# Kernel optimization log

Measured on AMD Instinct MI355X. Metric: run time of the kernel, lower is better.

## Reference

```python
import jax, jax.numpy as jnp
import numpy as np
import math

B, L, D = 4, 2048, 1024        # batch, x_len, x_dim
QKV, H = 64, 16                # qkv_dim, head_dim (number of heads)


def setup_inputs() -> dict:
    key = jax.random.key(0)
    ks = jax.random.split(key, 10)
    s = 1.0 / math.sqrt(D)
    return {
        "x": jax.random.normal(ks[0], (B, L, D), jnp.float32),
        "encoder_x": jax.random.normal(ks[1], (B, L, D), jnp.float32),
        "Wq": jax.random.normal(ks[2], (D, QKV * H), jnp.float32) * s,
        "bq": jax.random.normal(ks[3], (QKV * H,), jnp.float32) * 0.01,
        "Wk": jax.random.normal(ks[4], (D, QKV * H), jnp.float32) * s,
        "bk": jax.random.normal(ks[5], (QKV * H,), jnp.float32) * 0.01,
        "Wv": jax.random.normal(ks[6], (D, QKV * H), jnp.float32) * s,
        "bv": jax.random.normal(ks[7], (QKV * H,), jnp.float32) * 0.01,
        "Wo": jax.random.normal(ks[8], (QKV * H, D), jnp.float32) * s,
        "bo": jax.random.normal(ks[9], (D,), jnp.float32) * 0.01,
    }


def reference(x, encoder_x, Wq, bq, Wk, bk, Wv, bv, Wo, bo):
    # q,k from encoder_x; v from x  -> [B, L, H, QKV]
    q = (encoder_x @ Wq + bq).reshape(B, L, H, QKV)
    k = (encoder_x @ Wk + bk).reshape(B, L, H, QKV)
    v = (x @ Wv + bv).reshape(B, L, H, QKV)
    # explicit [B,H,L,L] score matrix + softmax over k (faithful to source)
    scores = jax.nn.softmax(
        jnp.einsum("bqhd,bkhd->bhqk", q, k) / math.sqrt(QKV), axis=-1
    )
    # faithful to source einsum 'bvhd,bhqk->bvhd': no shared contraction
    # index, so scores are summed over (q,k) and broadcast onto v per (b,h).
    attn = jnp.einsum("bvhd,bhqk->bvhd", v, scores).reshape(B, L, H * QKV)
    return attn @ Wo + bo
```

## Files before the change

### kernel.cpp

```cpp
#include <hip/hip_runtime.h>
#include <stdint.h>


typedef __attribute__((ext_vector_type(8))) short bf16x8;
typedef __attribute__((ext_vector_type(4))) float f32x4;

typedef __attribute__((address_space(1))) void as1_void;
typedef __attribute__((address_space(3))) void as3_void;
#define GLD16(g, s)                                                          \
  __builtin_amdgcn_global_load_lds((as1_void*)(g), (as3_void*)(s), 16, 0, 0)

__device__ __forceinline__ short f2bf(float f) {
  union { float f; uint32_t u; } v; v.f = f;
  uint32_t r = v.u + 0x7FFFu + ((v.u >> 16) & 1u);
  return (short)(r >> 16);
}

__device__ __forceinline__ bf16x8 pack8(f32x4 a, f32x4 b) {
  union { f32x4 f; uint32_t u[4]; } x, y;
  x.f = a; y.f = b;
#pragma unroll
  for (int t = 0; t < 4; ++t) x.u[t] += 0x8000u;
#pragma unroll
  for (int t = 0; t < 4; ++t) y.u[t] += 0x8000u;
  union { bf16x8 v; uint32_t u[4]; } o;
  o.u[0] = __builtin_amdgcn_perm(x.u[1], x.u[0], 0x07060302);
  o.u[1] = __builtin_amdgcn_perm(x.u[3], x.u[2], 0x07060302);
  o.u[2] = __builtin_amdgcn_perm(y.u[1], y.u[0], 0x07060302);
  o.u[3] = __builtin_amdgcn_perm(y.u[3], y.u[2], 0x07060302);
  return o.v;
}

__global__ __launch_bounds__(256) void cast_f32_bf16(
    const float* __restrict__ in, short* __restrict__ out, int n8) {
  int i = blockIdx.x * blockDim.x + threadIdx.x;
  if (i >= n8) return;
  const float4* p = (const float4*)in;
  float4 a = p[2 * (size_t)i], b = p[2 * (size_t)i + 1];
  bf16x8 o;
  o[0] = f2bf(a.x); o[1] = f2bf(a.y); o[2] = f2bf(a.z); o[3] = f2bf(a.w);
  o[4] = f2bf(b.x); o[5] = f2bf(b.y); o[6] = f2bf(b.z); o[7] = f2bf(b.w);
  *(bf16x8*)(out + 8 * (size_t)i) = o;
}

__global__ __launch_bounds__(256) void transpose_cast(
    const float* __restrict__ in, short* __restrict__ out, int n) {
  __shared__ float tile[64][65];
  const int br = blockIdx.y * 64, bc = blockIdx.x * 64;
  const int tid = threadIdx.x;
#pragma unroll
  for (int t = 0; t < 16; ++t) {
    int idx = t * 256 + tid;
    int r = idx >> 6, c = idx & 63;
    tile[r][c] = in[(size_t)(br + r) * n + bc + c];
  }
  __syncthreads();
#pragma unroll
  for (int t = 0; t < 16; ++t) {
    int idx = t * 256 + tid;
    int r = idx >> 6, c = idx & 63;
    out[(size_t)(bc + r) * n + br + c] = f2bf(tile[c][r]);
  }
}

__global__ __launch_bounds__(256) void bias_fuse(
    const float* __restrict__ bv, const float* __restrict__ Wo,
    const float* __restrict__ bo, float* __restrict__ biasc, int D, int N) {
  __shared__ float red[256];
  const int tid = threadIdx.x;
  const int nx = tid & 15, ky = tid >> 4;
  const int n = blockIdx.x * 16 + nx;
  float s = 0.f;
  for (int k = ky; k < D; k += 16)
    s += bv[k] * Wo[(size_t)k * N + n];
  red[tid] = s;
  __syncthreads();
#pragma unroll
  for (int st = 128; st >= 16; st >>= 1) {
    if (tid < st) red[tid] += red[tid + st];
    __syncthreads();
  }
  if (ky == 0) biasc[n] = 2048.0f * red[nx] + bo[n];
}

__global__ __launch_bounds__(256) void gemm_w(
    const short* __restrict__ Wot, const float* __restrict__ Wv,
    short* __restrict__ Wt, int N, int K) {
  constexpr int BK = 64;
  __shared__ __align__(16) short As[64 * BK];
  __shared__ __align__(16) float Bsf[64 * BK];
  const int tid = threadIdx.x, lane = tid & 63, wave = tid >> 6;
  const int bm = blockIdx.y * 64, bn = blockIdx.x * 64;
  const int wm = (wave >> 1) * 32, wn = (wave & 1) * 32;
  const int l15 = lane & 15, quad = lane >> 4;

  f32x4 acc[2][2];
#pragma unroll
  for (int i = 0; i < 2; ++i)
#pragma unroll
    for (int j = 0; j < 2; ++j) acc[i][j] = (f32x4){0.f, 0.f, 0.f, 0.f};

  const int ar = tid >> 3, ac8 = (tid & 7) ^ (ar & 7);
  const short* pa = Wot + (size_t)(bm + ar) * K + ac8 * 8;
  short* la = As + tid * 8;
  const int br = tid >> 4, bc4 = (tid & 15) ^ (br & 7);
  const float* pb = Wv + (size_t)(bn + br) * K + bc4 * 4;
  float* lb = Bsf + tid * 4;

  for (int kt = 0; kt < K; kt += BK) {
#pragma unroll
    for (int s = 0; s < 2; ++s) GLD16(pa + (size_t)(32 * s) * K, la + 2048 * s);
#pragma unroll
    for (int s = 0; s < 4; ++s) GLD16(pb + (size_t)(16 * s) * K, lb + 1024 * s);
    pa += BK; pb += BK;
    __syncthreads();
#pragma unroll
    for (int kk = 0; kk < 2; ++kk) {
      bf16x8 af[2], bfr[2];
#pragma unroll
      for (int i = 0; i < 2; ++i) {
        const int r = wm + i * 16 + l15;
        af[i] = *(const bf16x8*)(As + r * BK + ((kk * 4 + quad) ^ (r & 7)) * 8);
      }
#pragma unroll
      for (int j = 0; j < 2; ++j) {
        const int r = wn + j * 16 + l15;
        const int c4 = kk * 8 + quad * 2;
        f32x4 u0 = *(const f32x4*)(Bsf + (r * 16 + (c4 ^ (r & 7))) * 4);
        f32x4 u1 = *(const f32x4*)(Bsf + (r * 16 + ((c4 + 1) ^ (r & 7))) * 4);
        bfr[j] = pack8(u0, u1);
      }
#pragma unroll
      for (int i = 0; i < 2; ++i)
#pragma unroll
        for (int j = 0; j < 2; ++j)
          acc[i][j] = __builtin_amdgcn_mfma_f32_16x16x32_bf16(
              af[i], bfr[j], acc[i][j], 0, 0, 0);
    }
    __syncthreads();
  }
#pragma unroll
  for (int j = 0; j < 2; ++j) {
    const int col = bn + wn + j * 16 + l15;
#pragma unroll
    for (int i = 0; i < 2; ++i) {
      const int row0 = bm + wm + i * 16 + quad * 4;
#pragma unroll
      for (int r = 0; r < 4; ++r)
        Wt[(size_t)(row0 + r) * N + col] = f2bf(2048.f * acc[i][j][r]);
    }
  }
}

__global__ __launch_bounds__(256) void gemm_main(
    const short* __restrict__ A, const short* __restrict__ Bt,
    const float* __restrict__ bias, float* __restrict__ Out,
    int M, int N, int K) {
  constexpr int BK = 64;
  __shared__ __align__(16) char smem[24576];
  short* As = (short*)smem;
  short* Bs = (short*)(smem + 16384);
  const int tid = threadIdx.x, lane = tid & 63, wave = tid >> 6;
  const int b = blockIdx.x;
  const int bm = (b & 63) * 128;
  const int bn = (b >> 6) * 64;
  const int wm = (wave & 1) * 64, wn = (wave >> 1) * 32;
  const int l15 = lane & 15, quad = lane >> 4;

  f32x4 acc[4][2];
#pragma unroll
  for (int i = 0; i < 4; ++i)
#pragma unroll
    for (int j = 0; j < 2; ++j) acc[i][j] = (f32x4){0.f, 0.f, 0.f, 0.f};

  const int srow = tid >> 3, sc8 = (tid & 7) ^ (srow & 7);
  const short* pa = A + (size_t)(bm + srow) * K + sc8 * 8;
  const short* pb = Bt + (size_t)(bn + srow) * K + sc8 * 8;
  short* la = As + tid * 8;
  short* lb = Bs + tid * 8;

  for (int kt = 0; kt < K; kt += BK) {
#pragma unroll
    for (int s = 0; s < 4; ++s) GLD16(pa + (size_t)(32 * s) * K, la + 2048 * s);
#pragma unroll
    for (int s = 0; s < 2; ++s) GLD16(pb + (size_t)(32 * s) * K, lb + 2048 * s);
    pa += BK; pb += BK;
    __syncthreads();
#pragma unroll
    for (int kk = 0; kk < 2; ++kk) {
      bf16x8 af[4], bfr[2];
#pragma unroll
      for (int i = 0; i < 4; ++i) {
        const int r = wm + i * 16 + l15;
        af[i] = *(const bf16x8*)(As + r * BK + ((kk * 4 + quad) ^ (r & 7)) * 8);
      }
#pragma unroll
      for (int j = 0; j < 2; ++j) {
        const int r = wn + j * 16 + l15;
        bfr[j] = *(const bf16x8*)(Bs + r * BK + ((kk * 4 + quad) ^ (r & 7)) * 8);
      }
#pragma unroll
      for (int i = 0; i < 4; ++i)
#pragma unroll
        for (int j = 0; j < 2; ++j)
          acc[i][j] = __builtin_amdgcn_mfma_f32_16x16x32_bf16(
              af[i], bfr[j], acc[i][j], 0, 0, 0);
    }
    __syncthreads();
  }

  float* T = (float*)smem + wave * 576;
#pragma unroll
  for (int i = 0; i < 4; ++i) {
#pragma unroll
    for (int j = 0; j < 2; ++j) {
      const float bb = bias[bn + wn + j * 16 + l15];
#pragma unroll
      for (int r = 0; r < 4; ++r)
        T[(quad * 4 + r) * 36 + j * 16 + l15] = acc[i][j][r] + bb;
    }
#pragma unroll
    for (int c = 0; c < 2; ++c) {
      const int row = (lane >> 3) + 8 * c;
      f32x4 v = *(const f32x4*)(T + row * 36 + (lane & 7) * 4);
      *(f32x4*)(Out + (size_t)(bm + wm + i * 16 + row) * N + bn + wn +
                (lane & 7) * 4) = v;
    }
  }
}

extern "C" void kernel_launch(void* const* d_in, const int* in_sizes, int n_in,
                              void* d_out, int out_size, void* d_ws,
                              size_t ws_size, hipStream_t stream) {
  const float* x  = (const float*)d_in[0];
  const float* Wv = (const float*)d_in[6];
  const float* bv = (const float*)d_in[7];
  const float* Wo = (const float*)d_in[8];
  const float* bo = (const float*)d_in[9];
  float* out = (float*)d_out;

  constexpr int L = 2048, D = 1024, NO = 1024;
  constexpr int M = 4 * L;

  char* ws = (char*)d_ws;
  short* x_bf   = (short*)(ws);
  short* wot_bf = (short*)(ws + (16u << 20));
  short* wt_bf  = (short*)(ws + (18u << 20));
  float* biasc  = (float*)(ws + (20u << 20));

  cast_f32_bf16<<<(M * D / 8) / 256, 256, 0, stream>>>(x, x_bf, M * D / 8);
  transpose_cast<<<dim3(16, 16), 256, 0, stream>>>(Wo, wot_bf, NO);
  bias_fuse<<<NO / 16, 256, 0, stream>>>(bv, Wo, bo, biasc, D, NO);
  gemm_w<<<dim3(16, 16), 256, 0, stream>>>(wot_bf, Wv, wt_bf, NO, D);
  gemm_main<<<(M / 128) * (NO / 64), 256, 0, stream>>>(
      x_bf, wt_bf, biasc, out, M, NO, D);
}
```

Before: 185.2 us.

## Merge prep kernels into one launch and halve gemm_w tile height

Result: faster. 181.0 us (-2.3%).

```diff
diff --git a/kernel.cpp b/kernel.cpp
--- a/kernel.cpp
+++ b/kernel.cpp
@@ -31,74 +31,74 @@
   return o.v;
 }
 
-__global__ __launch_bounds__(256) void cast_f32_bf16(
-    const float* __restrict__ in, short* __restrict__ out, int n8) {
-  int i = blockIdx.x * blockDim.x + threadIdx.x;
-  if (i >= n8) return;
-  const float4* p = (const float4*)in;
-  float4 a = p[2 * (size_t)i], b = p[2 * (size_t)i + 1];
-  bf16x8 o;
-  o[0] = f2bf(a.x); o[1] = f2bf(a.y); o[2] = f2bf(a.z); o[3] = f2bf(a.w);
-  o[4] = f2bf(b.x); o[5] = f2bf(b.y); o[6] = f2bf(b.z); o[7] = f2bf(b.w);
-  *(bf16x8*)(out + 8 * (size_t)i) = o;
-}
-
-__global__ __launch_bounds__(256) void transpose_cast(
-    const float* __restrict__ in, short* __restrict__ out, int n) {
-  __shared__ float tile[64][65];
-  const int br = blockIdx.y * 64, bc = blockIdx.x * 64;
-  const int tid = threadIdx.x;
-#pragma unroll
-  for (int t = 0; t < 16; ++t) {
-    int idx = t * 256 + tid;
-    int r = idx >> 6, c = idx & 63;
-    tile[r][c] = in[(size_t)(br + r) * n + bc + c];
-  }
-  __syncthreads();
-#pragma unroll
-  for (int t = 0; t < 16; ++t) {
-    int idx = t * 256 + tid;
-    int r = idx >> 6, c = idx & 63;
-    out[(size_t)(bc + r) * n + br + c] = f2bf(tile[c][r]);
-  }
-}
-
-__global__ __launch_bounds__(256) void bias_fuse(
-    const float* __restrict__ bv, const float* __restrict__ Wo,
-    const float* __restrict__ bo, float* __restrict__ biasc, int D, int N) {
-  __shared__ float red[256];
-  const int tid = threadIdx.x;
-  const int nx = tid & 15, ky = tid >> 4;
-  const int n = blockIdx.x * 16 + nx;
-  float s = 0.f;
-  for (int k = ky; k < D; k += 16)
-    s += bv[k] * Wo[(size_t)k * N + n];
-  red[tid] = s;
-  __syncthreads();
-#pragma unroll
-  for (int st = 128; st >= 16; st >>= 1) {
-    if (tid < st) red[tid] += red[tid + st];
-    __syncthreads();
-  }
-  if (ky == 0) biasc[n] = 2048.0f * red[nx] + bo[n];
+__global__ __launch_bounds__(256) void prep(
+    const float* __restrict__ x, short* __restrict__ x_bf,
+    const float* __restrict__ Wo, short* __restrict__ wot,
+    const float* __restrict__ bv, const float* __restrict__ bo,
+    float* __restrict__ biasc) {
+  constexpr int N = 1024, D = 1024;
+  __shared__ union {
+    float tile[64][65];
+    float red[256];
+  } sm;
+  const int b = blockIdx.x, tid = threadIdx.x;
+
+  if (b < 4096) {
+    const int i = b * 256 + tid;
+    const float4* p = (const float4*)x;
+    float4 a = p[2 * (size_t)i], c = p[2 * (size_t)i + 1];
+    bf16x8 o;
+    o[0] = f2bf(a.x); o[1] = f2bf(a.y); o[2] = f2bf(a.z); o[3] = f2bf(a.w);
+    o[4] = f2bf(c.x); o[5] = f2bf(c.y); o[6] = f2bf(c.z); o[7] = f2bf(c.w);
+    *(bf16x8*)(x_bf + 8 * (size_t)i) = o;
+  } else if (b < 4352) {
+    const int b2 = b - 4096;
+    const int br = (b2 >> 4) * 64, bc = (b2 & 15) * 64;
+#pragma unroll
+    for (int t = 0; t < 16; ++t) {
+      int idx = t * 256 + tid;
+      int r = idx >> 6, c = idx & 63;
+      sm.tile[r][c] = Wo[(size_t)(br + r) * N + bc + c];
+    }
+    __syncthreads();
+#pragma unroll
+    for (int t = 0; t < 16; ++t) {
+      int idx = t * 256 + tid;
+      int r = idx >> 6, c = idx & 63;
+      wot[(size_t)(bc + r) * N + br + c] = f2bf(sm.tile[c][r]);
+    }
+  } else {
+    const int b3 = b - 4352;
+    const int nx = tid & 15, ky = tid >> 4;
+    const int n = b3 * 16 + nx;
+    float s = 0.f;
+    for (int k = ky; k < D; k += 16)
+      s += bv[k] * Wo[(size_t)k * N + n];
+    sm.red[tid] = s;
+    __syncthreads();
+#pragma unroll
+    for (int st = 128; st >= 16; st >>= 1) {
+      if (tid < st) sm.red[tid] += sm.red[tid + st];
+      __syncthreads();
+    }
+    if (ky == 0) biasc[n] = 2048.0f * sm.red[nx] + bo[n];
+  }
 }
 
 __global__ __launch_bounds__(256) void gemm_w(
     const short* __restrict__ Wot, const float* __restrict__ Wv,
     short* __restrict__ Wt, int N, int K) {
   constexpr int BK = 64;
-  __shared__ __align__(16) short As[64 * BK];
+  __shared__ __align__(16) short As[32 * BK];
   __shared__ __align__(16) float Bsf[64 * BK];
   const int tid = threadIdx.x, lane = tid & 63, wave = tid >> 6;
-  const int bm = blockIdx.y * 64, bn = blockIdx.x * 64;
-  const int wm = (wave >> 1) * 32, wn = (wave & 1) * 32;
+  const int bm = blockIdx.y * 32, bn = blockIdx.x * 64;
+  const int wm = (wave & 1) * 16, wn = (wave >> 1) * 32;
   const int l15 = lane & 15, quad = lane >> 4;
 
-  f32x4 acc[2][2];
-#pragma unroll
-  for (int i = 0; i < 2; ++i)
-#pragma unroll
-    for (int j = 0; j < 2; ++j) acc[i][j] = (f32x4){0.f, 0.f, 0.f, 0.f};
+  f32x4 acc[2];
+  acc[0] = (f32x4){0.f, 0.f, 0.f, 0.f};
+  acc[1] = (f32x4){0.f, 0.f, 0.f, 0.f};
 
   const int ar = tid >> 3, ac8 = (tid & 7) ^ (ar & 7);
   const short* pa = Wot + (size_t)(bm + ar) * K + ac8 * 8;
@@ -108,47 +108,35 @@
   float* lb = Bsf + tid * 4;
 
   for (int kt = 0; kt < K; kt += BK) {
-#pragma unroll
-    for (int s = 0; s < 2; ++s) GLD16(pa + (size_t)(32 * s) * K, la + 2048 * s);
+    GLD16(pa, la);
 #pragma unroll
     for (int s = 0; s < 4; ++s) GLD16(pb + (size_t)(16 * s) * K, lb + 1024 * s);
     pa += BK; pb += BK;
     __syncthreads();
 #pragma unroll
     for (int kk = 0; kk < 2; ++kk) {
-      bf16x8 af[2], bfr[2];
-#pragma unroll
-      for (int i = 0; i < 2; ++i) {
-        const int r = wm + i * 16 + l15;
-        af[i] = *(const bf16x8*)(As + r * BK + ((kk * 4 + quad) ^ (r & 7)) * 8);
+      const int r = wm + l15;
+      bf16x8 af =
+          *(const bf16x8*)(As + r * BK + ((kk * 4 + quad) ^ (r & 7)) * 8);
+#pragma unroll
+      for (int j = 0; j < 2; ++j) {
+        const int rn = wn + j * 16 + l15;
+        const int c4 = kk * 8 + quad * 2;
+        f32x4 u0 = *(const f32x4*)(Bsf + (rn * 16 + (c4 ^ (rn & 7))) * 4);
+        f32x4 u1 = *(const f32x4*)(Bsf + (rn * 16 + ((c4 + 1) ^ (rn & 7))) * 4);
+        acc[j] = __builtin_amdgcn_mfma_f32_16x16x32_bf16(af, pack8(u0, u1),
+                                                         acc[j], 0, 0, 0);
       }
-#pragma unroll
-      for (int j = 0; j < 2; ++j) {
-        const int r = wn + j * 16 + l15;
-        const int c4 = kk * 8 + quad * 2;
-        f32x4 u0 = *(const f32x4*)(Bsf + (r * 16 + (c4 ^ (r & 7))) * 4);
-        f32x4 u1 = *(const f32x4*)(Bsf + (r * 16 + ((c4 + 1) ^ (r & 7))) * 4);
-        bfr[j] = pack8(u0, u1);
-      }
-#pragma unroll
-      for (int i = 0; i < 2; ++i)
-#pragma unroll
-        for (int j = 0; j < 2; ++j)
-          acc[i][j] = __builtin_amdgcn_mfma_f32_16x16x32_bf16(
-              af[i], bfr[j], acc[i][j], 0, 0, 0);
     }
     __syncthreads();
   }
 #pragma unroll
   for (int j = 0; j < 2; ++j) {
     const int col = bn + wn + j * 16 + l15;
-#pragma unroll
-    for (int i = 0; i < 2; ++i) {
-      const int row0 = bm + wm + i * 16 + quad * 4;
-#pragma unroll
-      for (int r = 0; r < 4; ++r)
-        Wt[(size_t)(row0 + r) * N + col] = f2bf(2048.f * acc[i][j][r]);
-    }
+    const int row0 = bm + wm + quad * 4;
+#pragma unroll
+    for (int r = 0; r < 4; ++r)
+      Wt[(size_t)(row0 + r) * N + col] = f2bf(2048.f * acc[j][r]);
   }
 }
 
@@ -248,10 +236,8 @@
   short* wt_bf  = (short*)(ws + (18u << 20));
   float* biasc  = (float*)(ws + (20u << 20));
 
-  cast_f32_bf16<<<(M * D / 8) / 256, 256, 0, stream>>>(x, x_bf, M * D / 8);
-  transpose_cast<<<dim3(16, 16), 256, 0, stream>>>(Wo, wot_bf, NO);
-  bias_fuse<<<NO / 16, 256, 0, stream>>>(bv, Wo, bo, biasc, D, NO);
-  gemm_w<<<dim3(16, 16), 256, 0, stream>>>(wot_bf, Wv, wt_bf, NO, D);
+  prep<<<4416, 256, 0, stream>>>(x, x_bf, Wo, wot_bf, bv, bo, biasc);
+  gemm_w<<<dim3(16, 32), 256, 0, stream>>>(wot_bf, Wv, wt_bf, NO, D);
   gemm_main<<<(M / 128) * (NO / 64), 256, 0, stream>>>(
       x_bf, wt_bf, biasc, out, M, NO, D);
 }
```
